# Optimization experiments

Measured on AMD Instinct MI355X. Metric: run time of the kernel, lower is better.

## Reference

```python
import jax, jax.numpy as jnp
import numpy as np


def _ln(x, w, b, eps=1e-5):
    m = jnp.mean(x, -1, keepdims=True)
    v = jnp.mean((x - m) ** 2, -1, keepdims=True)
    return (x - m) / jnp.sqrt(v + eps) * w + b


def _l2norm(x, axis):
    n = jnp.sqrt(jnp.sum(x * x, axis=axis, keepdims=True))
    return x / jnp.maximum(n, 1e-12)


def _bilinear(img, gx, gy):
    # torch F.grid_sample, bilinear, align_corners=False, padding_mode='zeros'
    # img (B,C,H,W); gx, gy (B,N) in normalized [-1,1] coords -> out (B,C,N)
    B, C, H, W = img.shape
    x = ((gx + 1.0) * W - 1.0) * 0.5
    y = ((gy + 1.0) * H - 1.0) * 0.5
    x0f = jnp.floor(x)
    y0f = jnp.floor(y)
    wx1 = x - x0f
    wy1 = y - y0f
    x0 = x0f.astype(jnp.int32)
    y0 = y0f.astype(jnp.int32)
    imgf = img.reshape(B, C, H * W)

    def gat(xi, yi, wv):
        valid = (xi >= 0) & (xi < W) & (yi >= 0) & (yi < H)
        idx = jnp.clip(yi, 0, H - 1) * W + jnp.clip(xi, 0, W - 1)
        vals = jnp.take_along_axis(imgf, idx[:, None, :], axis=2)  # (B,C,N)
        return vals * (wv * valid)[:, None, :]

    return (gat(x0, y0, (1 - wx1) * (1 - wy1)) + gat(x0 + 1, y0, wx1 * (1 - wy1))
            + gat(x0, y0 + 1, (1 - wx1) * wy1) + gat(x0 + 1, y0 + 1, wx1 * wy1))


def _forward(xyz, g14d, v_feats, ext, intr, offsets,
             gate_w1, gate_b1, gate_w2, gate_b2,
             bn_w1, bn_b1, bn_w2, bn_b2, bn_ln_w, bn_ln_b,
             cw, cw2, hw, ln1_w, ln1_b, gw, gln_w, gln_b, mask):
    B, N, _ = xyz.shape
    BV, C, H, W = v_feats.shape
    V = BV // B
    vf = v_feats.reshape(B, V, C, H, W)
    gelu = lambda t: jax.nn.gelu(t, approximate=False)  # torch nn.GELU default

    # ---- PhysicsGatedProjection ----
    scale = jnp.clip(g14d[:, :, 4:7], 0.01, 10.0)
    opacity = jnp.clip(g14d[:, :, 11:12], 0.0, 1.0)
    gate = jax.nn.sigmoid(gelu(jnp.concatenate([scale, opacity], -1) @ gate_w1 + gate_b1) @ gate_w2 + gate_b2)  # (B,N,1)

    pts_homo = jnp.concatenate([xyz, jnp.ones((B, N, 1), xyz.dtype)], -1)  # (B,N,4)
    sum_f = jnp.zeros((B, N, 32), xyz.dtype)
    sum_m = jnp.zeros((B, N, 1), xyz.dtype)
    for v in range(V):  # small fixed view count
        cam = jnp.einsum('bij,bnj->bni', ext[:, v], pts_homo)      # (B,N,3)
        uvh = jnp.einsum('bij,bnj->bni', intr[:, v], cam)          # (B,N,3)
        depth = jnp.clip(uvh[:, :, 2:3], 1e-6, None)
        uv = uvh[:, :, :2] / depth
        grid = jnp.stack([2.0 * uv[:, :, 0] / (W * 14.0) - 1.0,
                          2.0 * uv[:, :, 1] / (H * 14.0) - 1.0], -1) + offsets  # (B,N,2)
        sampled = _bilinear(vf[:, v], grid[:, :, 0], grid[:, :, 1]).transpose(0, 2, 1)  # (B,N,C)
        h = gelu(sampled @ bn_w1 + bn_b1)
        v32 = _ln(h @ bn_w2 + bn_b2, bn_ln_w, bn_ln_b)             # (B,N,32)
        valid = (depth[:, :, 0] > 0.1) & jnp.all(jnp.abs(grid) <= 1.0, -1) & mask
        vm = valid[:, :, None].astype(xyz.dtype)
        sum_f = sum_f + v32 * gate * vm
        sum_m = sum_m + vm
    fused = sum_f / (sum_m + 1e-6)                                 # (B,N,32)

    # ---- NetVLADLoupe ----
    act = jax.nn.softmax(_ln(fused @ cw, ln1_w, ln1_b), -1)        # (B,N,K)
    act = act * mask[:, :, None].astype(fused.dtype)
    a_sum = jnp.sum(act, 1, keepdims=True)                         # (B,1,K)
    a = a_sum * cw2                                                # (B,D,K)
    vlad = jnp.einsum('bnk,bnd->bdk', act, fused) - a              # (B,D,K)
    vlad = _l2norm(vlad, axis=1)
    vlad = vlad.reshape(B, -1)
    vlad = _l2norm(vlad, axis=1)
    out = vlad @ hw                                                # (B,256)
    gates = jax.nn.sigmoid(_ln(out @ gw, gln_w, gln_b))
    return out * gates


def setup_inputs() -> dict:
    key = jax.random.key(0)
    ks = jax.random.split(key, 16)
    B, N, V, C, H, W = 4, 16384, 6, 384, 32, 32
    d = {}
    d['xyz'] = jax.random.normal(ks[0], (B, N, 3)) * 10.0
    d['g14d'] = jax.random.uniform(ks[1], (B, N, 14))
    d['v_feats'] = jax.random.normal(ks[2], (B * V, C, H, W))
    R = jnp.eye(3)[None, None] + 0.05 * jax.random.normal(ks[3], (B, V, 3, 3))
    t = jnp.concatenate([2.0 * jax.random.normal(ks[4], (B, V, 2, 1)),
                         20.0 + 5.0 * jax.random.uniform(ks[5], (B, V, 1, 1))], axis=2)
    d['ext'] = jnp.concatenate([R, t], -1)                          # (B,V,3,4)
    base_K = jnp.array([[200.0, 0.0, 224.0], [0.0, 200.0, 224.0], [0.0, 0.0, 1.0]])
    d['intr'] = base_K[None, None] + 2.0 * jax.random.normal(ks[6], (B, V, 3, 3)) * jnp.array([[1., 0., 1.], [0., 1., 1.], [0., 0., 0.]])
    d['offsets'] = jnp.zeros((B, N, 2))
    d['mask'] = jnp.ones((B, N), dtype=bool)
    # params
    d['gate_w1'] = jax.random.normal(ks[7], (4, 16)) * 0.5
    d['gate_b1'] = jnp.zeros((16,))
    d['gate_w2'] = jax.random.normal(ks[8], (16, 1)) * 0.25
    d['gate_b2'] = jnp.zeros((1,))
    d['bn_w1'] = jax.random.normal(ks[9], (384, 64)) / np.sqrt(384.0)
    d['bn_b1'] = jnp.zeros((64,))
    d['bn_w2'] = jax.random.normal(ks[10], (64, 32)) / 8.0
    d['bn_b2'] = jnp.zeros((32,))
    d['bn_ln_w'] = jnp.ones((32,))
    d['bn_ln_b'] = jnp.zeros((32,))
    d['cw'] = jax.random.normal(ks[11], (32, 64)) / np.sqrt(32.0)
    d['cw2'] = jax.random.normal(ks[12], (1, 32, 64)) / np.sqrt(32.0)
    d['hw'] = jax.random.normal(ks[13], (32 * 64, 256)) / np.sqrt(32.0)
    d['ln1_w'] = jnp.ones((64,))
    d['ln1_b'] = jnp.zeros((64,))
    d['gw'] = jax.random.normal(ks[14], (256, 256)) / 16.0
    d['gln_w'] = jnp.ones((256,))
    d['gln_b'] = jnp.zeros((256,))
    return d


def reference(xyz, g14d, v_feats, ext, intr, offsets, mask,
              gate_w1, gate_b1, gate_w2, gate_b2,
              bn_w1, bn_b1, bn_w2, bn_b2, bn_ln_w, bn_ln_b,
              cw, cw2, hw, ln1_w, ln1_b, gw, gln_w, gln_b):
    return _forward(xyz, g14d, v_feats, ext, intr, offsets,
                    gate_w1, gate_b1, gate_w2, gate_b2,
                    bn_w1, bn_b1, bn_w2, bn_b2, bn_ln_w, bn_ln_b,
                    cw, cw2, hw, ln1_w, ln1_b, gw, gln_w, gln_b, mask)
```

## Files before the change

kernel.cpp:

```cpp
#include <hip/hip_runtime.h>
#include <hip/hip_bf16.h>
#include <math.h>

#define B_ 4
#define N_ 16384
#define V_ 6
#define C_ 384
#define H_ 32
#define W_ 32
#define HW_ 1024
#define BN_ (B_ * N_)

__device__ __forceinline__ float gelu_f(float x){
  return 0.5f * x * (1.0f + erff(x * 0.70710678118654752440f));
}
__device__ __forceinline__ float sigmoid_f(float x){
  return 1.0f / (1.0f + expf(-x));
}
__device__ __forceinline__ float wsum64(float v){
  #pragma unroll
  for (int m = 1; m < 64; m <<= 1) v += __shfl_xor(v, m);
  return v;
}

__global__ __launch_bounds__(512) void k0_proj(
    const float* __restrict__ vf, const float* __restrict__ w1,
    float* __restrict__ proj)
{
  const int bv  = blockIdx.x >> 5;
  const int px0 = (blockIdx.x & 31) << 5;
  __shared__ float fs[64][32];
  const int t = threadIdx.x;
  const int j = t & 63;
  const int pg = t >> 6;
  const int sc = t >> 3, sq = t & 7;
  float acc0 = 0.f, acc1 = 0.f, acc2 = 0.f, acc3 = 0.f;

  for (int c0 = 0; c0 < C_; c0 += 64){
    const float4 sv = *(const float4*)&vf[((size_t)bv * C_ + c0 + sc) * HW_
                                          + px0 + sq * 4];
    __syncthreads();
    *(float4*)&fs[sc][sq * 4] = sv;
    __syncthreads();
    for (int c = 0; c < 64; ++c){
      const float w = w1[(c0 + c) * 64 + j];
      const float4 hv = *(const float4*)&fs[c][pg * 4];
      acc0 += hv.x * w;
      acc1 += hv.y * w;
      acc2 += hv.z * w;
      acc3 += hv.w * w;
    }
  }
  const size_t ob = ((size_t)bv * HW_ + px0 + pg * 4) * 64 + j;
  proj[ob]           = acc0;
  proj[ob + 64]      = acc1;
  proj[ob + 128]     = acc2;
  proj[ob + 192]     = acc3;
}

__global__ __launch_bounds__(64) void k1_fused(
    const float* __restrict__ xyz, const float* __restrict__ g14d,
    const float* __restrict__ ext, const float* __restrict__ intr,
    const float* __restrict__ offs, const unsigned char* __restrict__ mask,
    const float* __restrict__ gw1, const float* __restrict__ gb1,
    const float* __restrict__ gw2, const float* __restrict__ gb2,
    const float* __restrict__ proj,
    const float* __restrict__ b1, const float* __restrict__ w2,
    const float* __restrict__ b2, const float* __restrict__ lnw,
    const float* __restrict__ lnb, const float* __restrict__ cw,
    const float* __restrict__ ln1w, const float* __restrict__ ln1b,
    float* __restrict__ fused_out, float* __restrict__ act_out)
{
  const int p = blockIdx.x * 64 + threadIdx.x;
  const int b = p >> 14;
  const int bu = __builtin_amdgcn_readfirstlane(b);

  const float* g = g14d + (size_t)p * 14;
  float in0 = fminf(fmaxf(g[4],  0.01f), 10.f);
  float in1 = fminf(fmaxf(g[5],  0.01f), 10.f);
  float in2 = fminf(fmaxf(g[6],  0.01f), 10.f);
  float in3 = fminf(fmaxf(g[11], 0.0f),  1.f);
  float gacc = gb2[0];
  #pragma unroll
  for (int hh = 0; hh < 16; ++hh){
    float tv = gb1[hh] + in0 * gw1[hh] + in1 * gw1[16 + hh]
             + in2 * gw1[32 + hh] + in3 * gw1[48 + hh];
    gacc += gelu_f(tv) * gw2[hh];
  }
  const float gate = sigmoid_f(gacc);

  const float px = xyz[p * 3], py = xyz[p * 3 + 1], pz = xyz[p * 3 + 2];
  const float offx = offs[p * 2], offy = offs[p * 2 + 1];
  const float mval = mask[p] ? 1.f : 0.f;

  float sum_f[32];
  #pragma unroll
  for (int d = 0; d < 32; ++d) sum_f[d] = 0.f;
  float summ = 0.f;

  #pragma unroll 1
  for (int v = 0; v < V_; ++v){
    const float* E = ext  + (size_t)(bu * V_ + v) * 12;
    const float* I = intr + (size_t)(bu * V_ + v) * 9;
    float c0 = E[0]*px + E[1]*py + E[2]*pz + E[3];
    float c1 = E[4]*px + E[5]*py + E[6]*pz + E[7];
    float c2 = E[8]*px + E[9]*py + E[10]*pz + E[11];
    float u0 = I[0]*c0 + I[1]*c1 + I[2]*c2;
    float u1 = I[3]*c0 + I[4]*c1 + I[5]*c2;
    float u2 = I[6]*c0 + I[7]*c1 + I[8]*c2;
    float depth = fmaxf(u2, 1e-6f);
    float gx = 2.0f * (u0 / depth) / (W_ * 14.0f) - 1.0f + offx;
    float gy = 2.0f * (u1 / depth) / (H_ * 14.0f) - 1.0f + offy;
    float fx = ((gx + 1.0f) * W_ - 1.0f) * 0.5f;
    float fy = ((gy + 1.0f) * H_ - 1.0f) * 0.5f;
    fx = fminf(fmaxf(fx, -4.0f), 36.0f);
    fy = fminf(fmaxf(fy, -4.0f), 36.0f);
    float fx0 = floorf(fx), fy0 = floorf(fy);
    float wx = fx - fx0, wy = fy - fy0;
    int x0 = (int)fx0, y0 = (int)fy0;
    float v00 = (float)((x0 >= 0 && x0 < W_) && (y0 >= 0 && y0 < H_));
    float v10 = (float)((x0 + 1 >= 0 && x0 + 1 < W_) && (y0 >= 0 && y0 < H_));
    float v01 = (float)((x0 >= 0 && x0 < W_) && (y0 + 1 >= 0 && y0 + 1 < H_));
    float v11 = (float)((x0 + 1 >= 0 && x0 + 1 < W_) && (y0 + 1 >= 0 && y0 + 1 < H_));
    float vm = (depth > 0.1f && fabsf(gx) <= 1.0f && fabsf(gy) <= 1.0f) ? mval : 0.f;
    summ += vm;
    const int x0c = min(max(x0, 0), W_ - 1), x1c = min(max(x0 + 1, 0), W_ - 1);
    const int y0c = min(max(y0, 0), H_ - 1), y1c = min(max(y0 + 1, 0), H_ - 1);
    const float wv0 = (1.f - wx) * (1.f - wy) * v00;
    const float wv1 = wx * (1.f - wy) * v10;
    const float wv2 = (1.f - wx) * wy * v01;
    const float wv3 = wx * wy * v11;
    const float* pr = proj + (size_t)(bu * V_ + v) * (HW_ * 64);
    const float* t00p = pr + (y0c * W_ + x0c) * 64;
    const float* t10p = pr + (y0c * W_ + x1c) * 64;
    const float* t01p = pr + (y1c * W_ + x0c) * 64;
    const float* t11p = pr + (y1c * W_ + x1c) * 64;

    float y[32];
    #pragma unroll
    for (int d = 0; d < 32; ++d) y[d] = 0.f;
    #pragma unroll
    for (int q = 0; q < 16; ++q){
      const float4 a0 = *(const float4*)(t00p + q * 4);
      const float4 a1 = *(const float4*)(t10p + q * 4);
      const float4 a2 = *(const float4*)(t01p + q * 4);
      const float4 a3 = *(const float4*)(t11p + q * 4);
      float s0 = wv0 * a0.x; s0 += wv1 * a1.x; s0 += wv2 * a2.x; s0 += wv3 * a3.x;
      float s1 = wv0 * a0.y; s1 += wv1 * a1.y; s1 += wv2 * a2.y; s1 += wv3 * a3.y;
      float s2 = wv0 * a0.z; s2 += wv1 * a1.z; s2 += wv2 * a2.z; s2 += wv3 * a3.z;
      float s3 = wv0 * a0.w; s3 += wv1 * a1.w; s3 += wv2 * a2.w; s3 += wv3 * a3.w;
      const float h0 = gelu_f(s0 + b1[q * 4 + 0]);
      const float h1 = gelu_f(s1 + b1[q * 4 + 1]);
      const float h2 = gelu_f(s2 + b1[q * 4 + 2]);
      const float h3 = gelu_f(s3 + b1[q * 4 + 3]);
      #pragma unroll
      for (int d = 0; d < 32; ++d) y[d] += h0 * w2[(q * 4 + 0) * 32 + d];
      #pragma unroll
      for (int d = 0; d < 32; ++d) y[d] += h1 * w2[(q * 4 + 1) * 32 + d];
      #pragma unroll
      for (int d = 0; d < 32; ++d) y[d] += h2 * w2[(q * 4 + 2) * 32 + d];
      #pragma unroll
      for (int d = 0; d < 32; ++d) y[d] += h3 * w2[(q * 4 + 3) * 32 + d];
    }
    float mean = 0.f;
    #pragma unroll
    for (int d = 0; d < 32; ++d){ y[d] += b2[d]; mean += y[d]; }
    mean *= (1.f / 32.f);
    float var = 0.f;
    #pragma unroll
    for (int d = 0; d < 32; ++d){ float dv = y[d] - mean; var += dv * dv; }
    var *= (1.f / 32.f);
    const float rinv = rsqrtf(var + 1e-5f);
    #pragma unroll
    for (int d = 0; d < 32; ++d){
      float v32 = (y[d] - mean) * rinv * lnw[d] + lnb[d];
      sum_f[d] += v32 * gate * vm;
    }
  }

  const float rden = 1.f / (summ + 1e-6f);
  float fu[32];
  #pragma unroll
  for (int d = 0; d < 32; ++d) fu[d] = sum_f[d] * rden;
  #pragma unroll
  for (int q = 0; q < 8; ++q){
    float4 st;
    st.x = fu[q * 4 + 0]; st.y = fu[q * 4 + 1];
    st.z = fu[q * 4 + 2]; st.w = fu[q * 4 + 3];
    *(float4*)&fused_out[(size_t)p * 32 + q * 4] = st;
  }

  float z[64];
  #pragma unroll
  for (int k = 0; k < 64; ++k) z[k] = 0.f;
  #pragma unroll
  for (int d = 0; d < 32; ++d){
    const float fd = fu[d];
    #pragma unroll
    for (int k = 0; k < 64; ++k) z[k] += fd * cw[d * 64 + k];
  }
  float mean = 0.f;
  #pragma unroll
  for (int k = 0; k < 64; ++k) mean += z[k];
  mean *= (1.f / 64.f);
  float var = 0.f;
  #pragma unroll
  for (int k = 0; k < 64; ++k){ float dz = z[k] - mean; var += dz * dz; }
  var *= (1.f / 64.f);
  const float rinv = rsqrtf(var + 1e-5f);
  #pragma unroll
  for (int k = 0; k < 64; ++k) z[k] = (z[k] - mean) * rinv * ln1w[k] + ln1b[k];
  float mx = z[0];
  #pragma unroll
  for (int k = 1; k < 64; ++k) mx = fmaxf(mx, z[k]);
  float ssum = 0.f;
  #pragma unroll
  for (int k = 0; k < 64; ++k){ z[k] = expf(z[k] - mx); ssum += z[k]; }
  const float rs = 1.f / ssum;
  #pragma unroll
  for (int q = 0; q < 16; ++q){
    float4 st;
    st.x = (z[q * 4 + 0] * rs) * mval; st.y = (z[q * 4 + 1] * rs) * mval;
    st.z = (z[q * 4 + 2] * rs) * mval; st.w = (z[q * 4 + 3] * rs) * mval;
    *(float4*)&act_out[(size_t)p * 64 + q * 4] = st;
  }
}

__global__ __launch_bounds__(256) void k2_vlad(
    const float* __restrict__ fused, const float* __restrict__ act,
    float* __restrict__ vlad_acc, float* __restrict__ asum_acc)
{
  __shared__ float act_s[64][64];
  __shared__ float fu_s[64][32];
  const int b = blockIdx.x >> 6, seg = blockIdx.x & 63;
  const int n0 = seg * 256;
  const int t = threadIdx.x, k = t & 63, dg = t >> 6;
  float vacc[8];
  #pragma unroll
  for (int r = 0; r < 8; ++r) vacc[r] = 0.f;
  float asum = 0.f;

  for (int sc = 0; sc < 4; ++sc){
    int nb = n0 + sc * 64;
    #pragma unroll
    for (int i = 0; i < 16; ++i){
      int idx = t + i * 256;
      act_s[idx >> 6][idx & 63] =
        act[((size_t)((b << 14) + nb + (idx >> 6))) * 64 + (idx & 63)];
    }
    #pragma unroll
    for (int i = 0; i < 8; ++i){
      int idx = t + i * 256;
      fu_s[idx >> 5][idx & 31] =
        fused[((size_t)((b << 14) + nb + (idx >> 5))) * 32 + (idx & 31)];
    }
    __syncthreads();
    for (int i = 0; i < 64; ++i){
      float a = act_s[i][k];
      const float* fr = &fu_s[i][dg * 8];
      #pragma unroll
      for (int r = 0; r < 8; ++r) vacc[r] += a * fr[r];
      if (dg == 0) asum += a;
    }
    __syncthreads();
  }
  #pragma unroll
  for (int r = 0; r < 8; ++r)
    atomicAdd(&vlad_acc[b * 2048 + (dg * 8 + r) * 64 + k], vacc[r]);
  if (dg == 0) atomicAdd(&asum_acc[b * 64 + k], asum);
}

__global__ __launch_bounds__(256) void k3a_norm(
    const float* __restrict__ vlad_acc, const float* __restrict__ asum_acc,
    const float* __restrict__ cw2, float* __restrict__ vs1_g,
    float* __restrict__ ginv_g)
{
  const int b = blockIdx.x, t = threadIdx.x;
  __shared__ float vs[2048];
  __shared__ float denom[64];
  __shared__ float redA[4];
  #pragma unroll
  for (int i = 0; i < 8; ++i){
    int idx = t + i * 256;
    vs[idx] = vlad_acc[b * 2048 + idx]
            - asum_acc[b * 64 + (idx & 63)] * cw2[idx];
  }
  __syncthreads();
  if (t < 64){
    float ss = 0.f;
    #pragma unroll
    for (int dd = 0; dd < 32; ++dd){ float x = vs[dd * 64 + t]; ss += x * x; }
    denom[t] = fmaxf(sqrtf(ss), 1e-12f);
  }
  __syncthreads();
  float ls = 0.f;
  #pragma unroll
  for (int i = 0; i < 8; ++i){
    int idx = t + i * 256;
    float x = vs[idx] / denom[idx & 63];
    vs1_g[b * 2048 + idx] = x;
    ls += x * x;
  }
  ls = wsum64(ls);
  if ((t & 63) == 0) redA[t >> 6] = ls;
  __syncthreads();
  if (t == 0){
    float tot = redA[0] + redA[1] + redA[2] + redA[3];
    ginv_g[b] = 1.0f / fmaxf(sqrtf(tot), 1e-12f);
  }
}

__global__ __launch_bounds__(256) void k3b_hw(
    const float* __restrict__ vs1_g, const float* __restrict__ hw,
    float* __restrict__ out_acc)
{
  const int b = blockIdx.x >> 3, ks = blockIdx.x & 7;
  const int t = threadIdx.x;
  __shared__ float xs[256];
  xs[t] = vs1_g[b * 2048 + ks * 256 + t];
  __syncthreads();
  float acc = 0.f;
  #pragma unroll 4
  for (int i = 0; i < 256; ++i)
    acc += xs[i] * hw[(size_t)(ks * 256 + i) * 256 + t];
  atomicAdd(&out_acc[b * 256 + t], acc);
}

__global__ __launch_bounds__(256) void k3c_gate(
    const float* __restrict__ out_acc, const float* __restrict__ ginv_g,
    const float* __restrict__ gww, const float* __restrict__ glnw,
    const float* __restrict__ glnb, float* __restrict__ outp)
{
  const int b = blockIdx.x, t = threadIdx.x;
  __shared__ float out_s[256];
  __shared__ float redB[4], redC[4];
  const float ginv = ginv_g[b];
  const float o = out_acc[b * 256 + t] * ginv;
  out_s[t] = o;
  __syncthreads();
  float gp = 0.f;
  #pragma unroll 4
  for (int i = 0; i < 256; ++i) gp += out_s[i] * gww[i * 256 + t];
  float s1 = wsum64(gp);
  if ((t & 63) == 0) redB[t >> 6] = s1;
  __syncthreads();
  float mean = (redB[0] + redB[1] + redB[2] + redB[3]) * (1.f / 256.f);
  float dv = gp - mean;
  float s2 = wsum64(dv * dv);
  if ((t & 63) == 0) redC[t >> 6] = s2;
  __syncthreads();
  float var = (redC[0] + redC[1] + redC[2] + redC[3]) * (1.f / 256.f);
  float gt = sigmoid_f(dv * rsqrtf(var + 1e-5f) * glnw[t] + glnb[t]);
  outp[b * 256 + t] = o * gt;
}

extern "C" void kernel_launch(void* const* d_in, const int* in_sizes, int n_in,
                              void* d_out, int out_size, void* d_ws, size_t ws_size,
                              hipStream_t stream)
{
  (void)in_sizes; (void)n_in; (void)out_size; (void)ws_size;
  const float* xyz   = (const float*)d_in[0];
  const float* g14d  = (const float*)d_in[1];
  const float* vf    = (const float*)d_in[2];
  const float* ext   = (const float*)d_in[3];
  const float* intr  = (const float*)d_in[4];
  const float* offs  = (const float*)d_in[5];
  const unsigned char* mask = (const unsigned char*)d_in[6];
  const float* gw1   = (const float*)d_in[7];
  const float* gb1   = (const float*)d_in[8];
  const float* gw2   = (const float*)d_in[9];
  const float* gb2   = (const float*)d_in[10];
  const float* bnw1  = (const float*)d_in[11];
  const float* bnb1  = (const float*)d_in[12];
  const float* bnw2  = (const float*)d_in[13];
  const float* bnb2  = (const float*)d_in[14];
  const float* bnlnw = (const float*)d_in[15];
  const float* bnlnb = (const float*)d_in[16];
  const float* cw    = (const float*)d_in[17];
  const float* cw2   = (const float*)d_in[18];
  const float* hw    = (const float*)d_in[19];
  const float* ln1w  = (const float*)d_in[20];
  const float* ln1b  = (const float*)d_in[21];
  const float* gww   = (const float*)d_in[22];
  const float* glnw  = (const float*)d_in[23];
  const float* glnb  = (const float*)d_in[24];

  char* ws = (char*)d_ws;
  float* vlad_acc = (float*)(ws);
  float* asum_acc = (float*)(ws + 32768);
  float* out_acc  = (float*)(ws + 33792);
  float* ginv_g   = (float*)(ws + 37888);
  float* proj     = (float*)(ws + 38912);
  float* fusedb   = (float*)(ws + 6330368);
  float* actb     = (float*)(ws + 14718976);
  float* vs1_g    = (float*)(ws + 31496192);

  hipMemsetAsync(d_ws, 0, 37888, stream);
  k0_proj  <<<dim3(768),  dim3(512), 0, stream>>>(vf, bnw1, proj);
  k1_fused <<<dim3(1024), dim3(64),  0, stream>>>(
      xyz, g14d, ext, intr, offs, mask, gw1, gb1, gw2, gb2, proj,
      bnb1, bnw2, bnb2, bnlnw, bnlnb, cw, ln1w, ln1b, fusedb, actb);
  k2_vlad  <<<dim3(B_ * 64), dim3(256), 0, stream>>>(fusedb, actb, vlad_acc, asum_acc);
  k3a_norm <<<dim3(B_),   dim3(256), 0, stream>>>(vlad_acc, asum_acc, cw2,
                                                  vs1_g, ginv_g);
  k3b_hw   <<<dim3(32),   dim3(256), 0, stream>>>(vs1_g, hw, out_acc);
  k3c_gate <<<dim3(B_),   dim3(256), 0, stream>>>(out_acc, ginv_g, gww,
                                                  glnw, glnb, (float*)d_out);
}
```

Before: 415.2 us.

## Split fused point kernel into view-parallel pass and combine pass

The per-point fused kernel, which looped serially over all six views, is split in two. The first kernel handles the views in three groups of two, with one thread per point per group. It writes partial per-view contributions and mask sums to a workspace buffer. A second kernel computes the gate, sums the partials, normalizes, and runs the remaining per-point work. This triples the thread count to improve latency hiding and occupancy. The cost is an extra roughly 25MB intermediate written and read back, one more launch, and partial unrolling of the inner q loop. The workspace layout is reshuffled so fusedb reuses proj's region after proj is consumed.

```diff
diff --git a/kernel.cpp b/kernel.cpp
--- a/kernel.cpp
+++ b/kernel.cpp
@@ -58,48 +58,33 @@
   proj[ob + 192]     = acc3;
 }
 
-__global__ __launch_bounds__(64) void k1_fused(
-    const float* __restrict__ xyz, const float* __restrict__ g14d,
-    const float* __restrict__ ext, const float* __restrict__ intr,
-    const float* __restrict__ offs, const unsigned char* __restrict__ mask,
-    const float* __restrict__ gw1, const float* __restrict__ gb1,
-    const float* __restrict__ gw2, const float* __restrict__ gb2,
-    const float* __restrict__ proj,
+__global__ __launch_bounds__(256) void k1v_views(
+    const float* __restrict__ xyz, const float* __restrict__ ext,
+    const float* __restrict__ intr, const float* __restrict__ offs,
+    const unsigned char* __restrict__ mask, const float* __restrict__ proj,
     const float* __restrict__ b1, const float* __restrict__ w2,
     const float* __restrict__ b2, const float* __restrict__ lnw,
-    const float* __restrict__ lnb, const float* __restrict__ cw,
-    const float* __restrict__ ln1w, const float* __restrict__ ln1b,
-    float* __restrict__ fused_out, float* __restrict__ act_out)
-{
-  const int p = blockIdx.x * 64 + threadIdx.x;
+    const float* __restrict__ lnb,
+    float* __restrict__ contrib, float* __restrict__ vmsumb)
+{
+  const int t = blockIdx.x * 256 + threadIdx.x;
+  const int p = t & (BN_ - 1);
+  const int vp = __builtin_amdgcn_readfirstlane(t >> 16);
   const int b = p >> 14;
   const int bu = __builtin_amdgcn_readfirstlane(b);
-
-  const float* g = g14d + (size_t)p * 14;
-  float in0 = fminf(fmaxf(g[4],  0.01f), 10.f);
-  float in1 = fminf(fmaxf(g[5],  0.01f), 10.f);
-  float in2 = fminf(fmaxf(g[6],  0.01f), 10.f);
-  float in3 = fminf(fmaxf(g[11], 0.0f),  1.f);
-  float gacc = gb2[0];
-  #pragma unroll
-  for (int hh = 0; hh < 16; ++hh){
-    float tv = gb1[hh] + in0 * gw1[hh] + in1 * gw1[16 + hh]
-             + in2 * gw1[32 + hh] + in3 * gw1[48 + hh];
-    gacc += gelu_f(tv) * gw2[hh];
-  }
-  const float gate = sigmoid_f(gacc);
 
   const float px = xyz[p * 3], py = xyz[p * 3 + 1], pz = xyz[p * 3 + 2];
   const float offx = offs[p * 2], offy = offs[p * 2 + 1];
   const float mval = mask[p] ? 1.f : 0.f;
 
-  float sum_f[32];
-  #pragma unroll
-  for (int d = 0; d < 32; ++d) sum_f[d] = 0.f;
-  float summ = 0.f;
+  float c[32];
+  #pragma unroll
+  for (int d = 0; d < 32; ++d) c[d] = 0.f;
+  float vmsum = 0.f;
 
   #pragma unroll 1
-  for (int v = 0; v < V_; ++v){
+  for (int j = 0; j < 2; ++j){
+    const int v = vp * 2 + j;
     const float* E = ext  + (size_t)(bu * V_ + v) * 12;
     const float* I = intr + (size_t)(bu * V_ + v) * 9;
     float c0 = E[0]*px + E[1]*py + E[2]*pz + E[3];
@@ -123,7 +108,7 @@
     float v01 = (float)((x0 >= 0 && x0 < W_) && (y0 + 1 >= 0 && y0 + 1 < H_));
     float v11 = (float)((x0 + 1 >= 0 && x0 + 1 < W_) && (y0 + 1 >= 0 && y0 + 1 < H_));
     float vm = (depth > 0.1f && fabsf(gx) <= 1.0f && fabsf(gy) <= 1.0f) ? mval : 0.f;
-    summ += vm;
+    vmsum += vm;
     const int x0c = min(max(x0, 0), W_ - 1), x1c = min(max(x0 + 1, 0), W_ - 1);
     const int y0c = min(max(y0, 0), H_ - 1), y1c = min(max(y0 + 1, 0), H_ - 1);
     const float wv0 = (1.f - wx) * (1.f - wy) * v00;
@@ -139,7 +124,7 @@
     float y[32];
     #pragma unroll
     for (int d = 0; d < 32; ++d) y[d] = 0.f;
-    #pragma unroll
+    #pragma unroll 4
     for (int q = 0; q < 16; ++q){
       const float4 a0 = *(const float4*)(t00p + q * 4);
       const float4 a1 = *(const float4*)(t10p + q * 4);
@@ -174,14 +159,61 @@
     #pragma unroll
     for (int d = 0; d < 32; ++d){
       float v32 = (y[d] - mean) * rinv * lnw[d] + lnb[d];
-      sum_f[d] += v32 * gate * vm;
-    }
-  }
-
+      c[d] += v32 * vm;
+    }
+  }
+
+  float* crow = contrib + ((size_t)vp * BN_ + p) * 32;
+  #pragma unroll
+  for (int q = 0; q < 8; ++q){
+    float4 st;
+    st.x = c[q * 4 + 0]; st.y = c[q * 4 + 1];
+    st.z = c[q * 4 + 2]; st.w = c[q * 4 + 3];
+    *(float4*)&crow[q * 4] = st;
+  }
+  vmsumb[(size_t)vp * BN_ + p] = vmsum;
+}
+
+__global__ __launch_bounds__(256) void k1c_combine(
+    const float* __restrict__ g14d, const unsigned char* __restrict__ mask,
+    const float* __restrict__ gw1, const float* __restrict__ gb1,
+    const float* __restrict__ gw2, const float* __restrict__ gb2,
+    const float* __restrict__ contrib, const float* __restrict__ vmsumb,
+    const float* __restrict__ cw, const float* __restrict__ ln1w,
+    const float* __restrict__ ln1b,
+    float* __restrict__ fused_out, float* __restrict__ act_out)
+{
+  const int p = blockIdx.x * 256 + threadIdx.x;
+
+  const float* g = g14d + (size_t)p * 14;
+  float in0 = fminf(fmaxf(g[4],  0.01f), 10.f);
+  float in1 = fminf(fmaxf(g[5],  0.01f), 10.f);
+  float in2 = fminf(fmaxf(g[6],  0.01f), 10.f);
+  float in3 = fminf(fmaxf(g[11], 0.0f),  1.f);
+  float gacc = gb2[0];
+  #pragma unroll
+  for (int hh = 0; hh < 16; ++hh){
+    float tv = gb1[hh] + in0 * gw1[hh] + in1 * gw1[16 + hh]
+             + in2 * gw1[32 + hh] + in3 * gw1[48 + hh];
+    gacc += gelu_f(tv) * gw2[hh];
+  }
+  const float gate = sigmoid_f(gacc);
+  const float mval = mask[p] ? 1.f : 0.f;
+
+  const float summ = (vmsumb[p] + vmsumb[BN_ + p]) + vmsumb[2 * BN_ + p];
   const float rden = 1.f / (summ + 1e-6f);
+
   float fu[32];
   #pragma unroll
-  for (int d = 0; d < 32; ++d) fu[d] = sum_f[d] * rden;
+  for (int q = 0; q < 8; ++q){
+    const float4 c0 = *(const float4*)&contrib[((size_t)0 * BN_ + p) * 32 + q * 4];
+    const float4 c1 = *(const float4*)&contrib[((size_t)1 * BN_ + p) * 32 + q * 4];
+    const float4 c2 = *(const float4*)&contrib[((size_t)2 * BN_ + p) * 32 + q * 4];
+    fu[q * 4 + 0] = (((c0.x + c1.x) + c2.x) * gate) * rden;
+    fu[q * 4 + 1] = (((c0.y + c1.y) + c2.y) * gate) * rden;
+    fu[q * 4 + 2] = (((c0.z + c1.z) + c2.z) * gate) * rden;
+    fu[q * 4 + 3] = (((c0.w + c1.w) + c2.w) * gate) * rden;
+  }
   #pragma unroll
   for (int q = 0; q < 8; ++q){
     float4 st;
@@ -391,19 +423,25 @@
   float* out_acc  = (float*)(ws + 33792);
   float* ginv_g   = (float*)(ws + 37888);
   float* proj     = (float*)(ws + 38912);
-  float* fusedb   = (float*)(ws + 6330368);
-  float* actb     = (float*)(ws + 14718976);
-  float* vs1_g    = (float*)(ws + 31496192);
+  float* fusedb   = (float*)(ws + 38912);
+  float* contrib  = (float*)(ws + 38912 + 8388608);
+  float* vmsumb   = (float*)(ws + 38912 + 8388608 + 25165824);
+  float* actb     = (float*)(ws + 38912 + 8388608 + 25165824 + 786432);
+  float* vs1_g    = (float*)(ws + 38912 + 8388608 + 25165824 + 786432
+                             + 16777216);
 
   hipMemsetAsync(d_ws, 0, 37888, stream);
-  k0_proj  <<<dim3(768),  dim3(512), 0, stream>>>(vf, bnw1, proj);
-  k1_fused <<<dim3(1024), dim3(64),  0, stream>>>(
-      xyz, g14d, ext, intr, offs, mask, gw1, gb1, gw2, gb2, proj,
-      bnb1, bnw2, bnb2, bnlnw, bnlnb, cw, ln1w, ln1b, fusedb, actb);
-  k2_vlad  <<<dim3(B_ * 64), dim3(256), 0, stream>>>(fusedb, actb, vlad_acc, asum_acc);
-  k3a_norm <<<dim3(B_),   dim3(256), 0, stream>>>(vlad_acc, asum_acc, cw2,
-                                                  vs1_g, ginv_g);
-  k3b_hw   <<<dim3(32),   dim3(256), 0, stream>>>(vs1_g, hw, out_acc);
-  k3c_gate <<<dim3(B_),   dim3(256), 0, stream>>>(out_acc, ginv_g, gww,
-                                                  glnw, glnb, (float*)d_out);
-}
+  k0_proj    <<<dim3(768), dim3(512), 0, stream>>>(vf, bnw1, proj);
+  k1v_views  <<<dim3(768), dim3(256), 0, stream>>>(
+      xyz, ext, intr, offs, mask, proj,
+      bnb1, bnw2, bnb2, bnlnw, bnlnb, contrib, vmsumb);
+  k1c_combine<<<dim3(256), dim3(256), 0, stream>>>(
+      g14d, mask, gw1, gb1, gw2, gb2, contrib, vmsumb,
+      cw, ln1w, ln1b, fusedb, actb);
+  k2_vlad    <<<dim3(B_ * 64), dim3(256), 0, stream>>>(fusedb, actb, vlad_acc, asum_acc);
+  k3a_norm   <<<dim3(B_),  dim3(256), 0, stream>>>(vlad_acc, asum_acc, cw2,
+                                                   vs1_g, ginv_g);
+  k3b_hw     <<<dim3(32),  dim3(256), 0, stream>>>(vs1_g, hw, out_acc);
+  k3c_gate   <<<dim3(B_),  dim3(256), 0, stream>>>(out_acc, ginv_g, gww,
+                                                   glnw, glnb, (float*)d_out);
+}
```

Result: faster. 383.5 us (-7.6%).
